# Performance work log

Hardware: AMD Instinct MI355X
Metric: run time of the kernel (lower is better)

The kernel has to match this reference:

```python
import jax, jax.numpy as jnp
import numpy as np

B, S, D, H = 4, 2048, 512, 8
DH = D // H


def setup_inputs() -> dict:
    key = jax.random.key(0)
    ks = jax.random.split(key, 7)
    scale = 1.0 / np.sqrt(DH)  # mimic nn.Linear init magnitude
    return {
        "x": jax.random.normal(ks[0], (B, S, D), dtype=jnp.float32),
        "Wq": jax.random.normal(ks[1], (H, DH, DH), dtype=jnp.float32) * scale,
        "bq": jax.random.normal(ks[2], (H, DH), dtype=jnp.float32) * scale,
        "Wk": jax.random.normal(ks[3], (H, DH, DH), dtype=jnp.float32) * scale,
        "bk": jax.random.normal(ks[4], (H, DH), dtype=jnp.float32) * scale,
        "Wv": jax.random.normal(ks[5], (H, DH, DH), dtype=jnp.float32) * scale,
        "bv": jax.random.normal(ks[6], (H, DH), dtype=jnp.float32) * scale,
    }


def reference(x, Wq, bq, Wk, bk, Wv, bv):
    # x: [B, S, D] -> per-head slices [B, S, H, DH] (contiguous chunks, as in torch slicing)
    xh = x.reshape(B, S, H, DH)
    # nn.Linear: y = x @ W.T + b, per head. Wq[h] is [out, in].
    q = jnp.einsum("bshd,hed->bshe", xh, Wq) + bq  # [B, S, H, DH]
    k = jnp.einsum("bshd,hed->bshe", xh, Wk) + bk
    v = jnp.einsum("bshd,hed->bshe", xh, Wv) + bv
    scores = jnp.einsum("bshe,bthe->bhst", q, k) / jnp.sqrt(jnp.float32(DH))  # [B, H, S, S]
    attn = jax.nn.softmax(scores, axis=-1)
    out = jnp.einsum("bhst,bthe->bshe", attn, v)  # [B, S, H, DH]
    return out.reshape(B, S, D)  # hstack of head outputs == concat along feature dim
```

## Files before the change

kernel.cpp:

```cpp
#include <hip/hip_runtime.h>
#include <math.h>

#define B_ 4
#define S_ 2048
#define D_ 512
#define H_ 8
#define DH_ 64
#define BH_ (B_*H_)
#define SCALE 0.1803368801111243f

typedef __attribute__((ext_vector_type(4)))  float f32x4;
typedef __attribute__((ext_vector_type(16))) float f32x16;
typedef __attribute__((ext_vector_type(8)))  short bf16x8;
typedef __attribute__((ext_vector_type(4)))  uint  u32x4;

__device__ inline uint rnepk(float a, float b) {
    uint ua = __builtin_bit_cast(uint, a), ub = __builtin_bit_cast(uint, b);
    ua += 0x7FFFu + ((ua >> 16) & 1u);
    ub += 0x7FFFu + ((ub >> 16) & 1u);
    return (ua >> 16) | (ub & 0xFFFF0000u);
}
__device__ inline uint truncpk(float lo, float hi) {
    return __builtin_amdgcn_perm(__builtin_bit_cast(uint, hi),
                                 __builtin_bit_cast(uint, lo), 0x07060302u);
}
__device__ inline f32x16 zero16() {
    f32x16 z;
    #pragma unroll
    for (int i = 0; i < 16; ++i) z[i] = 0.f;
    return z;
}
__device__ inline bf16x8 pack8(f32x4 a, f32x4 c) {
    u32x4 u;
    u.x = rnepk(a[0], a[1]); u.y = rnepk(a[2], a[3]);
    u.z = rnepk(c[0], c[1]); u.w = rnepk(c[2], c[3]);
    return __builtin_bit_cast(bf16x8, u);
}

#if __has_builtin(__builtin_amdgcn_permlane32_swap)
__device__ inline void lane32swap(uint& a, uint& b) {
    typedef __attribute__((ext_vector_type(2))) uint u32x2;
    u32x2 r = __builtin_amdgcn_permlane32_swap(a, b, false, false);
    a = r.x; b = r.y;
}
#else
__device__ inline void lane32swap(uint& a, uint& b) {
    const int l5 = (threadIdx.x & 63) >> 5;
    uint send = l5 ? a : b;
    uint recv = __shfl_xor(send, 32);
    uint an = l5 ? recv : a;
    uint bn = l5 ? b : recv;
    a = an; b = bn;
}
#endif

__global__ __launch_bounds__(256, 2)
void qkv_mfma(const float* __restrict__ x,
              const float* __restrict__ Wq, const float* __restrict__ bq,
              const float* __restrict__ Wk, const float* __restrict__ bk,
              const float* __restrict__ Wv, const float* __restrict__ bv,
              ushort* __restrict__ Qb, ushort* __restrict__ Kb,
              ushort* __restrict__ Vtg)
{
    const int bh = blockIdx.x, b = bh >> 3, h = bh & 7;
    const int s0 = blockIdx.y * 128;
    const int tid = threadIdx.x;
    const int w = tid >> 6, lane = tid & 63, l31 = lane & 31, l5 = lane >> 5;

    __shared__ __align__(16) ushort bnc[4][2560];
    ushort* mybnc = &bnc[w][0];

    const int srow = w * 32 + l31;
    const float* xr = x + ((size_t)(b * S_ + s0 + srow)) * D_ + h * DH_;
    bf16x8 xf[4];
    #pragma unroll
    for (int st = 0; st < 4; ++st) {
        f32x4 a = *(const f32x4*)(xr + st * 16 + l5 * 8);
        f32x4 c = *(const f32x4*)(xr + st * 16 + l5 * 8 + 4);
        xf[st] = pack8(a, c);
    }

    const float* Wm[3] = {Wq, Wk, Wv};
    #pragma unroll
    for (int mat = 0; mat < 3; ++mat) {
        bf16x8 wf[2][4];
        #pragma unroll
        for (int et = 0; et < 2; ++et) {
            const float* wr = Wm[mat] + h * DH_ * DH_ + (et * 32 + l31) * DH_;
            #pragma unroll
            for (int st = 0; st < 4; ++st) {
                f32x4 a = *(const f32x4*)(wr + st * 16 + l5 * 8);
                f32x4 c = *(const f32x4*)(wr + st * 16 + l5 * 8 + 4);
                wf[et][st] = pack8(a, c);
            }
        }

        if (mat < 2) {
            const float* bias = mat ? bk : bq;
            #pragma unroll
            for (int et = 0; et < 2; ++et) {
                f32x16 acc = zero16();
                #pragma unroll
                for (int st = 0; st < 4; ++st)
                    acc = __builtin_amdgcn_mfma_f32_32x32x16_bf16(wf[et][st], xf[st], acc, 0, 0, 0);
                #pragma unroll
                for (int rg = 0; rg < 4; ++rg) {
                    float4 b4 = *(const float4*)(bias + h * DH_ + et * 32 + rg * 8 + l5 * 4);
                    float v0 = acc[rg * 4 + 0] + b4.x;
                    float v1 = acc[rg * 4 + 1] + b4.y;
                    float v2 = acc[rg * 4 + 2] + b4.z;
                    float v3 = acc[rg * 4 + 3] + b4.w;
                    if (mat == 0) { v0 *= SCALE; v1 *= SCALE; v2 *= SCALE; v3 *= SCALE; }
                    uint2 pk;
                    pk.x = rnepk(v0, v1); pk.y = rnepk(v2, v3);
                    *(uint2*)(mybnc + l31 * 72 + et * 32 + rg * 8 + l5 * 4) = pk;
                }
            }
            ushort* Og = mat ? Kb : Qb;
            #pragma unroll
            for (int i = 0; i < 4; ++i) {
                const int slot = lane + 64 * i;
                const int r = slot >> 3, c = slot & 7;
                uint4 v = *(const uint4*)(mybnc + r * 72 + c * 8);
                *(uint4*)(Og + ((size_t)(bh * S_ + s0 + w * 32 + r)) * DH_ + c * 8) = v;
            }
        } else {
            #pragma unroll
            for (int et = 0; et < 2; ++et) {
                f32x16 acc = zero16();
                #pragma unroll
                for (int st = 0; st < 4; ++st)
                    acc = __builtin_amdgcn_mfma_f32_32x32x16_bf16(xf[st], wf[et][st], acc, 0, 0, 0);
                const float bb = bv[h * DH_ + et * 32 + l31];
                #pragma unroll
                for (int rg = 0; rg < 4; ++rg) {
                    uint2 pk;
                    pk.x = rnepk(acc[rg * 4 + 0] + bb, acc[rg * 4 + 1] + bb);
                    pk.y = rnepk(acc[rg * 4 + 2] + bb, acc[rg * 4 + 3] + bb);
                    *(uint2*)(mybnc + (et * 32 + l31) * 40 + rg * 8 + l5 * 4) = pk;
                }
            }
            #pragma unroll
            for (int i = 0; i < 4; ++i) {
                const int slot = lane + 64 * i;
                const int r = slot >> 2, c = slot & 3;
                uint4 v = *(const uint4*)(mybnc + r * 40 + c * 8);
                *(uint4*)(Vtg + ((size_t)(bh * DH_ + r)) * S_ + s0 + w * 32 + c * 8) = v;
            }
        }
    }
}

__global__ __launch_bounds__(256, 2)
void flash_mfma(const ushort* __restrict__ Qb, const ushort* __restrict__ Kb,
                const ushort* __restrict__ Vtg, float* __restrict__ out)
{
    const int blk = blockIdx.x;
    const int bh = blk & 31, qblk = blk >> 5;
    const int b = bh >> 3, h = bh & 7;
    const int tid = threadIdx.x;
    const int w = tid >> 6, lane = tid & 63, l31 = lane & 31, l5 = lane >> 5;

    __shared__ __align__(16) ushort lds_u[17408];

    const int q0 = qblk * 128 + w * 32;
    bf16x8 qf[4];
    #pragma unroll
    for (int st = 0; st < 4; ++st)
        qf[st] = *(const bf16x8*)(Qb + ((size_t)(bh * S_ + q0 + l31)) * DH_
                                  + st * 16 + l5 * 8);

    f32x16 O[2];
    O[0] = zero16(); O[1] = zero16();
    float lsum = 0.f;

    const ushort* kg = Kb + (size_t)bh * S_ * DH_;
    const ushort* vg = Vtg + (size_t)bh * DH_ * S_;
    const int sr0 = tid >> 3, sc = tid & 7, sr1 = sr0 + 32;
    const int swz0 = (sc ^ (sr0 & 7)) * 8, swz1 = (sc ^ (sr1 & 7)) * 8;

    {
        uint4 k0 = *(const uint4*)(kg + (size_t)sr0 * DH_ + sc * 8);
        uint4 k1 = *(const uint4*)(kg + (size_t)sr1 * DH_ + sc * 8);
        uint4 v0 = *(const uint4*)(vg + (size_t)sr0 * S_ + sc * 8);
        uint4 v1 = *(const uint4*)(vg + (size_t)sr1 * S_ + sc * 8);
        *(uint4*)(lds_u + sr0 * 64 + swz0) = k0;
        *(uint4*)(lds_u + sr1 * 64 + swz1) = k1;
        *(uint4*)(lds_u + 8192 + sr0 * 64 + swz0) = v0;
        *(uint4*)(lds_u + 8192 + sr1 * 64 + swz1) = v1;
    }

    for (int kt = 0; kt < 32; ++kt) {
        __syncthreads();
        const int cur = kt & 1, nxt = cur ^ 1;
        uint4 kv0, kv1, vv0, vv1;
        if (kt < 31) {
            const size_t ko = (size_t)(kt + 1) * 64 * DH_;
            const int vo = (kt + 1) * 64;
            kv0 = *(const uint4*)(kg + ko + (size_t)sr0 * DH_ + sc * 8);
            kv1 = *(const uint4*)(kg + ko + (size_t)sr1 * DH_ + sc * 8);
            vv0 = *(const uint4*)(vg + (size_t)sr0 * S_ + vo + sc * 8);
            vv1 = *(const uint4*)(vg + (size_t)sr1 * S_ + vo + sc * 8);
        }
        const ushort* ksb = lds_u + cur * 4096;
        const ushort* vsb = lds_u + 8192 + cur * 4096;

        bf16x8 pf[4];
        #pragma unroll
        for (int g = 0; g < 2; ++g) {
            const int key = g * 32 + l31;
            bf16x8 kf[4];
            #pragma unroll
            for (int st = 0; st < 4; ++st)
                kf[st] = *(const bf16x8*)(ksb + key * 64 + (((st * 2 + l5) ^ (key & 7)) * 8));
            f32x16 sc_ = zero16();
            #pragma unroll
            for (int st = 0; st < 4; ++st)
                sc_ = __builtin_amdgcn_mfma_f32_32x32x16_bf16(kf[st], qf[st], sc_, 0, 0, 0);
            uint pr[8];
            #pragma unroll
            for (int rg = 0; rg < 4; ++rg) {
                float p0 = __builtin_amdgcn_exp2f(sc_[rg * 4 + 0]);
                float p1 = __builtin_amdgcn_exp2f(sc_[rg * 4 + 1]);
                float p2 = __builtin_amdgcn_exp2f(sc_[rg * 4 + 2]);
                float p3 = __builtin_amdgcn_exp2f(sc_[rg * 4 + 3]);
                lsum += (p0 + p1) + (p2 + p3);
                pr[2 * rg + 0] = truncpk(p0, p1);
                pr[2 * rg + 1] = truncpk(p2, p3);
            }
            #pragma unroll
            for (int p = 0; p < 2; ++p) {
                lane32swap(pr[4 * p + 0], pr[4 * p + 2]);
                lane32swap(pr[4 * p + 1], pr[4 * p + 3]);
                u32x4 u; u.x = pr[4 * p + 0]; u.y = pr[4 * p + 1];
                u.z = pr[4 * p + 2]; u.w = pr[4 * p + 3];
                pf[g * 2 + p] = __builtin_bit_cast(bf16x8, u);
            }
        }

        #pragma unroll
        for (int dht = 0; dht < 2; ++dht) {
            const int dh = dht * 32 + l31;
            bf16x8 vf[4];
            #pragma unroll
            for (int st = 0; st < 4; ++st)
                vf[st] = *(const bf16x8*)(vsb + dh * 64 + (((st * 2 + l5) ^ (dh & 7)) * 8));
            #pragma unroll
            for (int st = 0; st < 4; ++st)
                O[dht] = __builtin_amdgcn_mfma_f32_32x32x16_bf16(vf[st], pf[st], O[dht], 0, 0, 0);
        }

        if (kt < 31) {
            ushort* kn = lds_u + nxt * 4096;
            ushort* vn = lds_u + 8192 + nxt * 4096;
            *(uint4*)(kn + sr0 * 64 + swz0) = kv0;
            *(uint4*)(kn + sr1 * 64 + swz1) = kv1;
            *(uint4*)(vn + sr0 * 64 + swz0) = vv0;
            *(uint4*)(vn + sr1 * 64 + swz1) = vv1;
        }
    }

    lsum += __shfl_xor(lsum, 32);
    const float linv = 1.0f / lsum;
    #pragma unroll
    for (int dht = 0; dht < 2; ++dht)
        #pragma unroll
        for (int i = 0; i < 16; ++i) O[dht][i] *= linv;

    __syncthreads();
    float* ob = (float*)lds_u + w * (32 * 68);
    #pragma unroll
    for (int dht = 0; dht < 2; ++dht)
        #pragma unroll
        for (int rg = 0; rg < 4; ++rg) {
            f32x4 v4;
            v4[0] = O[dht][rg * 4 + 0];
            v4[1] = O[dht][rg * 4 + 1];
            v4[2] = O[dht][rg * 4 + 2];
            v4[3] = O[dht][rg * 4 + 3];
            *(f32x4*)(ob + l31 * 68 + dht * 32 + rg * 8 + l5 * 4) = v4;
        }
    #pragma unroll
    for (int i = 0; i < 8; ++i) {
        const int slot = lane + 64 * i;
        const int r = slot >> 4, c = slot & 15;
        f32x4 v = *(const f32x4*)(ob + r * 68 + c * 4);
        *(f32x4*)(out + ((size_t)(b * S_ + q0 + r)) * D_ + h * DH_ + c * 4) = v;
    }
}

extern "C" void kernel_launch(void* const* d_in, const int* in_sizes, int n_in,
                              void* d_out, int out_size, void* d_ws, size_t ws_size,
                              hipStream_t stream) {
    const float* x  = (const float*)d_in[0];
    const float* Wq = (const float*)d_in[1];
    const float* bq = (const float*)d_in[2];
    const float* Wk = (const float*)d_in[3];
    const float* bk = (const float*)d_in[4];
    const float* Wv = (const float*)d_in[5];
    const float* bv = (const float*)d_in[6];
    float* outp = (float*)d_out;

    ushort* Qb  = (ushort*)d_ws;
    ushort* Kb  = Qb + (size_t)BH_ * S_ * DH_;
    ushort* Vtg = Kb + (size_t)BH_ * S_ * DH_;

    qkv_mfma<<<dim3(BH_, S_ / 128), 256, 0, stream>>>(x, Wq, bq, Wk, bk, Wv, bv,
                                                      Qb, Kb, Vtg);
    flash_mfma<<<dim3(32 * 16), 256, 0, stream>>>(Qb, Kb, Vtg, outp);
}
```

Baseline: 134.8 us.

## Fuse QKV projection into flash attention kernel with per-head atomic barrier

Merges the projection kernel and the attention kernel into one launch. Each block computes K and V for its 128-row slice, publishes them to global memory, and signals a per-head counter. It then computes Q directly into MFMA registers using lane swaps, skipping the Q round trip through global memory, and spin-waits until all 16 blocks of its head have finished. This removes one kernel launch and the Q store and reload. In exchange it adds a memset, an inter-block spin barrier that depends on all 512 blocks being co-resident, and some serialization while blocks wait.

```diff
diff --git a/kernel.cpp b/kernel.cpp
--- a/kernel.cpp
+++ b/kernel.cpp
@@ -55,121 +55,154 @@
 #endif
 
 __global__ __launch_bounds__(256, 2)
-void qkv_mfma(const float* __restrict__ x,
-              const float* __restrict__ Wq, const float* __restrict__ bq,
-              const float* __restrict__ Wk, const float* __restrict__ bk,
-              const float* __restrict__ Wv, const float* __restrict__ bv,
-              ushort* __restrict__ Qb, ushort* __restrict__ Kb,
-              ushort* __restrict__ Vtg)
-{
-    const int bh = blockIdx.x, b = bh >> 3, h = bh & 7;
-    const int s0 = blockIdx.y * 128;
-    const int tid = threadIdx.x;
-    const int w = tid >> 6, lane = tid & 63, l31 = lane & 31, l5 = lane >> 5;
-
-    __shared__ __align__(16) ushort bnc[4][2560];
-    ushort* mybnc = &bnc[w][0];
-
-    const int srow = w * 32 + l31;
-    const float* xr = x + ((size_t)(b * S_ + s0 + srow)) * D_ + h * DH_;
-    bf16x8 xf[4];
-    #pragma unroll
-    for (int st = 0; st < 4; ++st) {
-        f32x4 a = *(const f32x4*)(xr + st * 16 + l5 * 8);
-        f32x4 c = *(const f32x4*)(xr + st * 16 + l5 * 8 + 4);
-        xf[st] = pack8(a, c);
-    }
-
-    const float* Wm[3] = {Wq, Wk, Wv};
-    #pragma unroll
-    for (int mat = 0; mat < 3; ++mat) {
-        bf16x8 wf[2][4];
-        #pragma unroll
-        for (int et = 0; et < 2; ++et) {
-            const float* wr = Wm[mat] + h * DH_ * DH_ + (et * 32 + l31) * DH_;
-            #pragma unroll
-            for (int st = 0; st < 4; ++st) {
-                f32x4 a = *(const f32x4*)(wr + st * 16 + l5 * 8);
-                f32x4 c = *(const f32x4*)(wr + st * 16 + l5 * 8 + 4);
-                wf[et][st] = pack8(a, c);
-            }
-        }
-
-        if (mat < 2) {
-            const float* bias = mat ? bk : bq;
-            #pragma unroll
-            for (int et = 0; et < 2; ++et) {
-                f32x16 acc = zero16();
-                #pragma unroll
-                for (int st = 0; st < 4; ++st)
-                    acc = __builtin_amdgcn_mfma_f32_32x32x16_bf16(wf[et][st], xf[st], acc, 0, 0, 0);
-                #pragma unroll
-                for (int rg = 0; rg < 4; ++rg) {
-                    float4 b4 = *(const float4*)(bias + h * DH_ + et * 32 + rg * 8 + l5 * 4);
-                    float v0 = acc[rg * 4 + 0] + b4.x;
-                    float v1 = acc[rg * 4 + 1] + b4.y;
-                    float v2 = acc[rg * 4 + 2] + b4.z;
-                    float v3 = acc[rg * 4 + 3] + b4.w;
-                    if (mat == 0) { v0 *= SCALE; v1 *= SCALE; v2 *= SCALE; v3 *= SCALE; }
-                    uint2 pk;
-                    pk.x = rnepk(v0, v1); pk.y = rnepk(v2, v3);
-                    *(uint2*)(mybnc + l31 * 72 + et * 32 + rg * 8 + l5 * 4) = pk;
-                }
-            }
-            ushort* Og = mat ? Kb : Qb;
-            #pragma unroll
-            for (int i = 0; i < 4; ++i) {
-                const int slot = lane + 64 * i;
-                const int r = slot >> 3, c = slot & 7;
-                uint4 v = *(const uint4*)(mybnc + r * 72 + c * 8);
-                *(uint4*)(Og + ((size_t)(bh * S_ + s0 + w * 32 + r)) * DH_ + c * 8) = v;
-            }
-        } else {
-            #pragma unroll
-            for (int et = 0; et < 2; ++et) {
-                f32x16 acc = zero16();
-                #pragma unroll
-                for (int st = 0; st < 4; ++st)
-                    acc = __builtin_amdgcn_mfma_f32_32x32x16_bf16(xf[st], wf[et][st], acc, 0, 0, 0);
-                const float bb = bv[h * DH_ + et * 32 + l31];
-                #pragma unroll
-                for (int rg = 0; rg < 4; ++rg) {
-                    uint2 pk;
-                    pk.x = rnepk(acc[rg * 4 + 0] + bb, acc[rg * 4 + 1] + bb);
-                    pk.y = rnepk(acc[rg * 4 + 2] + bb, acc[rg * 4 + 3] + bb);
-                    *(uint2*)(mybnc + (et * 32 + l31) * 40 + rg * 8 + l5 * 4) = pk;
-                }
-            }
-            #pragma unroll
-            for (int i = 0; i < 4; ++i) {
-                const int slot = lane + 64 * i;
-                const int r = slot >> 2, c = slot & 3;
-                uint4 v = *(const uint4*)(mybnc + r * 40 + c * 8);
-                *(uint4*)(Vtg + ((size_t)(bh * DH_ + r)) * S_ + s0 + w * 32 + c * 8) = v;
-            }
-        }
-    }
-}
-
-__global__ __launch_bounds__(256, 2)
-void flash_mfma(const ushort* __restrict__ Qb, const ushort* __restrict__ Kb,
-                const ushort* __restrict__ Vtg, float* __restrict__ out)
+void msa_fused(const float* __restrict__ x,
+               const float* __restrict__ Wq, const float* __restrict__ bq,
+               const float* __restrict__ Wk, const float* __restrict__ bk,
+               const float* __restrict__ Wv, const float* __restrict__ bv,
+               ushort* __restrict__ Kb, ushort* __restrict__ Vtg,
+               uint* __restrict__ cnt, float* __restrict__ out)
 {
     const int blk = blockIdx.x;
     const int bh = blk & 31, qblk = blk >> 5;
     const int b = bh >> 3, h = bh & 7;
     const int tid = threadIdx.x;
     const int w = tid >> 6, lane = tid & 63, l31 = lane & 31, l5 = lane >> 5;
+    const int s0 = qblk * 128;
 
     __shared__ __align__(16) ushort lds_u[17408];
-
-    const int q0 = qblk * 128 + w * 32;
+    ushort* mybnc = lds_u + w * 2560;
+
+    const int srow = w * 32 + l31;
+    const float* xr = x + ((size_t)(b * S_ + s0 + srow)) * D_ + h * DH_;
+    bf16x8 xf[4];
+    #pragma unroll
+    for (int st = 0; st < 4; ++st) {
+        f32x4 a = *(const f32x4*)(xr + st * 16 + l5 * 8);
+        f32x4 c = *(const f32x4*)(xr + st * 16 + l5 * 8 + 4);
+        xf[st] = pack8(a, c);
+    }
+
+    {
+        bf16x8 wf[2][4];
+        #pragma unroll
+        for (int et = 0; et < 2; ++et) {
+            const float* wr = Wk + h * DH_ * DH_ + (et * 32 + l31) * DH_;
+            #pragma unroll
+            for (int st = 0; st < 4; ++st)
+                wf[et][st] = pack8(*(const f32x4*)(wr + st * 16 + l5 * 8),
+                                   *(const f32x4*)(wr + st * 16 + l5 * 8 + 4));
+        }
+        #pragma unroll
+        for (int et = 0; et < 2; ++et) {
+            f32x16 acc = zero16();
+            #pragma unroll
+            for (int st = 0; st < 4; ++st)
+                acc = __builtin_amdgcn_mfma_f32_32x32x16_bf16(wf[et][st], xf[st], acc, 0, 0, 0);
+            #pragma unroll
+            for (int rg = 0; rg < 4; ++rg) {
+                float4 b4 = *(const float4*)(bk + h * DH_ + et * 32 + rg * 8 + l5 * 4);
+                uint2 pk;
+                pk.x = rnepk(acc[rg * 4 + 0] + b4.x, acc[rg * 4 + 1] + b4.y);
+                pk.y = rnepk(acc[rg * 4 + 2] + b4.z, acc[rg * 4 + 3] + b4.w);
+                *(uint2*)(mybnc + l31 * 72 + et * 32 + rg * 8 + l5 * 4) = pk;
+            }
+        }
+        #pragma unroll
+        for (int i = 0; i < 4; ++i) {
+            const int slot = lane + 64 * i;
+            const int r = slot >> 3, c = slot & 7;
+            uint4 v = *(const uint4*)(mybnc + r * 72 + c * 8);
+            *(uint4*)(Kb + ((size_t)(bh * S_ + s0 + w * 32 + r)) * DH_ + c * 8) = v;
+        }
+    }
+
+    {
+        bf16x8 wf[2][4];
+        #pragma unroll
+        for (int et = 0; et < 2; ++et) {
+            const float* wr = Wv + h * DH_ * DH_ + (et * 32 + l31) * DH_;
+            #pragma unroll
+            for (int st = 0; st < 4; ++st)
+                wf[et][st] = pack8(*(const f32x4*)(wr + st * 16 + l5 * 8),
+                                   *(const f32x4*)(wr + st * 16 + l5 * 8 + 4));
+        }
+        #pragma unroll
+        for (int et = 0; et < 2; ++et) {
+            f32x16 acc = zero16();
+            #pragma unroll
+            for (int st = 0; st < 4; ++st)
+                acc = __builtin_amdgcn_mfma_f32_32x32x16_bf16(xf[st], wf[et][st], acc, 0, 0, 0);
+            const float bb = bv[h * DH_ + et * 32 + l31];
+            #pragma unroll
+            for (int rg = 0; rg < 4; ++rg) {
+                uint2 pk;
+                pk.x = rnepk(acc[rg * 4 + 0] + bb, acc[rg * 4 + 1] + bb);
+                pk.y = rnepk(acc[rg * 4 + 2] + bb, acc[rg * 4 + 3] + bb);
+                *(uint2*)(mybnc + (et * 32 + l31) * 40 + rg * 8 + l5 * 4) = pk;
+            }
+        }
+        #pragma unroll
+        for (int i = 0; i < 4; ++i) {
+            const int slot = lane + 64 * i;
+            const int r = slot >> 2, c = slot & 3;
+            uint4 v = *(const uint4*)(mybnc + r * 40 + c * 8);
+            *(uint4*)(Vtg + ((size_t)(bh * DH_ + r)) * S_ + s0 + w * 32 + c * 8) = v;
+        }
+    }
+
+    __syncthreads();
+    if (tid == 0) {
+        __threadfence();
+        __hip_atomic_fetch_add(&cnt[bh], 1u, __ATOMIC_RELAXED,
+                               __HIP_MEMORY_SCOPE_AGENT);
+    }
+
     bf16x8 qf[4];
-    #pragma unroll
-    for (int st = 0; st < 4; ++st)
-        qf[st] = *(const bf16x8*)(Qb + ((size_t)(bh * S_ + q0 + l31)) * DH_
-                                  + st * 16 + l5 * 8);
-
+    {
+        bf16x8 wf[2][4];
+        #pragma unroll
+        for (int et = 0; et < 2; ++et) {
+            const float* wr = Wq + h * DH_ * DH_ + (et * 32 + l31) * DH_;
+            #pragma unroll
+            for (int st = 0; st < 4; ++st)
+                wf[et][st] = pack8(*(const f32x4*)(wr + st * 16 + l5 * 8),
+                                   *(const f32x4*)(wr + st * 16 + l5 * 8 + 4));
+        }
+        #pragma unroll
+        for (int et = 0; et < 2; ++et) {
+            f32x16 acc = zero16();
+            #pragma unroll
+            for (int st = 0; st < 4; ++st)
+                acc = __builtin_amdgcn_mfma_f32_32x32x16_bf16(wf[et][st], xf[st], acc, 0, 0, 0);
+            uint qr[8];
+            #pragma unroll
+            for (int rg = 0; rg < 4; ++rg) {
+                float4 b4 = *(const float4*)(bq + h * DH_ + et * 32 + rg * 8 + l5 * 4);
+                qr[2 * rg + 0] = rnepk((acc[rg * 4 + 0] + b4.x) * SCALE,
+                                       (acc[rg * 4 + 1] + b4.y) * SCALE);
+                qr[2 * rg + 1] = rnepk((acc[rg * 4 + 2] + b4.z) * SCALE,
+                                       (acc[rg * 4 + 3] + b4.w) * SCALE);
+            }
+            #pragma unroll
+            for (int p = 0; p < 2; ++p) {
+                lane32swap(qr[4 * p + 0], qr[4 * p + 2]);
+                lane32swap(qr[4 * p + 1], qr[4 * p + 3]);
+                u32x4 u; u.x = qr[4 * p + 0]; u.y = qr[4 * p + 1];
+                u.z = qr[4 * p + 2]; u.w = qr[4 * p + 3];
+                qf[et * 2 + p] = __builtin_bit_cast(bf16x8, u);
+            }
+        }
+    }
+
+    if (tid == 0) {
+        while (__hip_atomic_load(&cnt[bh], __ATOMIC_RELAXED,
+                                 __HIP_MEMORY_SCOPE_AGENT) < 16u)
+            __builtin_amdgcn_s_sleep(2);
+    }
+    __syncthreads();
+    __threadfence();
+
+    const int q0 = s0 + w * 32;
     f32x16 O[2];
     O[0] = zero16(); O[1] = zero16();
     float lsum = 0.f;
@@ -301,11 +334,11 @@
     const float* bv = (const float*)d_in[6];
     float* outp = (float*)d_out;
 
-    ushort* Qb  = (ushort*)d_ws;
-    ushort* Kb  = Qb + (size_t)BH_ * S_ * DH_;
+    ushort* Kb  = (ushort*)d_ws;
     ushort* Vtg = Kb + (size_t)BH_ * S_ * DH_;
-
-    qkv_mfma<<<dim3(BH_, S_ / 128), 256, 0, stream>>>(x, Wq, bq, Wk, bk, Wv, bv,
-                                                      Qb, Kb, Vtg);
-    flash_mfma<<<dim3(32 * 16), 256, 0, stream>>>(Qb, Kb, Vtg, outp);
-}
+    uint*   cnt = (uint*)((char*)d_ws + 16u * 1024 * 1024);
+
+    hipMemsetAsync(cnt, 0, 32 * sizeof(uint), stream);
+    msa_fused<<<dim3(512), 256, 0, stream>>>(x, Wq, bq, Wk, bk, Wv, bv,
+                                             Kb, Vtg, cnt, outp);
+}
```

After: 188.1 us. +39.5%, slower.
